# Kernel tuning notes

Measured on AMD Instinct MI355X. Metric: run time of the kernel, lower is better.

The kernel has to match this reference:

```python
import jax, jax.numpy as jnp
import numpy as np

N, D, DFF, H, L = 98280, 192, 384, 8, 36
S = N // L  # 2730 sets per partition
HD = D // H
EPS = 1e-5


def _ln(x, g, b):
    m = x.mean(-1, keepdims=True)
    v = ((x - m) ** 2).mean(-1, keepdims=True)
    return (x - m) * jax.lax.rsqrt(v + EPS) * g + b


def _mha(q, k, v, Wqkv, bqkv, Wo, bo, mask):
    # q,k,v: (S, L, D); mask: (S, L), True = padded key
    Wq, Wk, Wv = jnp.split(Wqkv, 3, axis=0)
    bq, bk, bv = jnp.split(bqkv, 3)
    qh = (q @ Wq.T + bq).reshape(S, L, H, HD)
    kh = (k @ Wk.T + bk).reshape(S, L, H, HD)
    vh = (v @ Wv.T + bv).reshape(S, L, H, HD)
    scores = jnp.einsum('slhd,smhd->shlm', qh, kh) / np.sqrt(HD).astype(np.float32)
    scores = jnp.where(mask[:, None, None, :], -1e9, scores)
    attn = jax.nn.softmax(scores, axis=-1)
    out = jnp.einsum('shlm,smhd->slhd', attn, vh).reshape(S, L, D)
    return out @ Wo.T + bo


def _layer(x, pos, inds, mask, Wqkv, bqkv, Wo, bo, W1, b1, W2, b2,
           g1, be1, g2, be2, gn, bn):
    identity = x
    sf = x[inds]                 # gather voxels into sets: (S, L, D)
    qk = sf + pos[inds]          # pos added to q and k only (value = sf)
    src2 = _mha(qk, qk, sf, Wqkv, bqkv, Wo, bo, mask)
    flat = inds.reshape(-1)
    # torch.unique(return_inverse) + flip + scatter == take FIRST occurrence
    # of each voxel id; .at[].min is deterministic under duplicates.
    perm = jnp.full((N,), flat.shape[0], jnp.int32).at[flat].min(
        jnp.arange(flat.shape[0], dtype=jnp.int32))
    src2 = src2.reshape(-1, D)[perm]   # scatter back: (N, D)
    x = _ln(x + src2, g1, be1)
    ff = jnp.maximum(x @ W1.T + b1, 0.0) @ W2.T + b2
    x = _ln(x + ff, g2, be2)
    return _ln(x + identity, gn, bn)   # DSVT_EncoderLayer residual norm


def reference(src, inds0, inds1, mask0, mask1, pos0, pos1,
              Wqkv, bqkv, Wo, bo, W1, b1, W2, b2,
              g1, be1, g2, be2, gn, bn, block_id):
    inds = (inds0, inds1)
    masks = (mask0, mask1)
    pos = (pos0, pos1)
    out = src
    for i in range(2):  # two set partitions within the shift (shift_id = block_id % 2)
        out = _layer(out, pos[i], inds[i], masks[i],
                     Wqkv[i], bqkv[i], Wo[i], bo[i],
                     W1[i], b1[i], W2[i], b2[i],
                     g1[i], be1[i], g2[i], be2[i], gn[i], bn[i])
    return out


def setup_inputs():
    key = jax.random.key(0)
    ks = jax.random.split(key, 16)
    sd = 0.02
    return {
        "src": jax.random.normal(ks[0], (N, D), jnp.float32),
        "inds0": jax.random.permutation(ks[1], N).reshape(S, L).astype(jnp.int32),
        "inds1": jax.random.permutation(ks[2], N).reshape(S, L).astype(jnp.int32),
        "mask0": jnp.zeros((S, L), bool),
        "mask1": jnp.zeros((S, L), bool),
        "pos0": jax.random.normal(ks[3], (N, D), jnp.float32),
        "pos1": jax.random.normal(ks[4], (N, D), jnp.float32),
        "Wqkv": sd * jax.random.normal(ks[5], (2, 3 * D, D), jnp.float32),
        "bqkv": jnp.zeros((2, 3 * D), jnp.float32),
        "Wo": sd * jax.random.normal(ks[6], (2, D, D), jnp.float32),
        "bo": jnp.zeros((2, D), jnp.float32),
        "W1": sd * jax.random.normal(ks[7], (2, DFF, D), jnp.float32),
        "b1": jnp.zeros((2, DFF), jnp.float32),
        "W2": sd * jax.random.normal(ks[8], (2, D, DFF), jnp.float32),
        "b2": jnp.zeros((2, D), jnp.float32),
        "g1": jnp.ones((2, D), jnp.float32),
        "be1": jnp.zeros((2, D), jnp.float32),
        "g2": jnp.ones((2, D), jnp.float32),
        "be2": jnp.zeros((2, D), jnp.float32),
        "gn": jnp.ones((2, D), jnp.float32),
        "bn": jnp.zeros((2, D), jnp.float32),
        "block_id": 0,
    }
```

## Files before the change

### kernel.cpp

```cpp
#include <hip/hip_runtime.h>
#include <stdint.h>

#define NVOX   98280
#define S_SETS 2730
#define L_SET  36
#define D_MODEL 192
#define D_FF    384
#define N_HEADS 8
#define H_DIM   24

using s16x8 = __attribute__((ext_vector_type(8))) short;
using s16x4 = __attribute__((ext_vector_type(4))) short;
using f32x4 = __attribute__((ext_vector_type(4))) float;

__device__ __forceinline__ float bf2f(unsigned short h) {
    unsigned u = ((unsigned)h) << 16;
    return __builtin_bit_cast(float, u);
}
__device__ __forceinline__ unsigned short f2bf(float f) {
    unsigned u = __builtin_bit_cast(unsigned, f);
    u += 0x7FFF + ((u >> 16) & 1);
    return (unsigned short)(u >> 16);
}

__global__ __launch_bounds__(256)
void convert_f32_bf16(const float* __restrict__ src, short* __restrict__ dst, int n)
{
    int i = blockIdx.x * 256 + threadIdx.x;
    if (i < n) dst[i] = (short)f2bf(src[i]);
}

__global__ __launch_bounds__(256)
void gather_kernel(const float* __restrict__ x, const float* __restrict__ pos,
                   const int* __restrict__ inds,
                   short* __restrict__ qk, short* __restrict__ sf)
{
    int f = blockIdx.x * 4 + (threadIdx.x >> 6);
    int lane = threadIdx.x & 63;
    if (lane >= 48) return;
    int v = inds[f];
    float4 a = *(const float4*)(x + (size_t)v * D_MODEL + lane * 4);
    float4 p = *(const float4*)(pos + (size_t)v * D_MODEL + lane * 4);
    s16x4 q, s;
    q[0] = (short)f2bf(a.x + p.x); q[1] = (short)f2bf(a.y + p.y);
    q[2] = (short)f2bf(a.z + p.z); q[3] = (short)f2bf(a.w + p.w);
    s[0] = (short)f2bf(a.x); s[1] = (short)f2bf(a.y);
    s[2] = (short)f2bf(a.z); s[3] = (short)f2bf(a.w);
    *(s16x4*)(qk + (size_t)f * D_MODEL + lane * 4) = q;
    *(s16x4*)(sf + (size_t)f * D_MODEL + lane * 4) = s;
}

__global__ __launch_bounds__(512, 4)
void qkv_direct(const short* __restrict__ qk, const short* __restrict__ sf,
                const short* __restrict__ W, const float* __restrict__ bias,
                short* __restrict__ C, int n)
{
    __shared__ char Bs[36864];
    const int bx = blockIdx.x;
    const int sec = bx >> 1, half = bx & 1;
    const int colOff = sec * 192 + half * 96;
    const short* Ap = (sec == 2) ? sf : qk;
    const short* Wp = W + (size_t)colOff * 192;
    const int rowBase = blockIdx.y * 128;
    const int tid = threadIdx.x;

    #pragma unroll
    for (int t = tid; t < 2304; t += 512) {
        int row = t / 24, c8 = t % 24;
        s16x8 v = *(const s16x8*)(Wp + (size_t)row * 192 + c8 * 8);
        *(s16x8*)(Bs + row * 384 + ((c8 * 16) ^ ((row & 7) << 4))) = v;
    }
    __syncthreads();

    const int wid = tid >> 6, lane = tid & 63;
    const int lr = lane & 15, kb = lane >> 4;
    const int arow = rowBase + wid * 16 + lr;
    const bool rv = arow < n;
    const short* Arow = Ap + (size_t)arow * 192 + kb * 8;

    f32x4 acc[6] = {};
    #pragma unroll
    for (int ks = 0; ks < 6; ++ks) {
        s16x8 a = {};
        if (rv) a = *(const s16x8*)(Arow + ks * 32);
        s16x8 b[6];
        #pragma unroll
        for (int fj = 0; fj < 6; ++fj) {
            int row = fj * 16 + lr;
            b[fj] = *(const s16x8*)(Bs + row * 384 + ((ks * 64 + kb * 16) ^ ((row & 7) << 4)));
        }
        #pragma unroll
        for (int fj = 0; fj < 6; ++fj)
            acc[fj] = __builtin_amdgcn_mfma_f32_16x16x32_bf16(a, b[fj], acc[fj], 0, 0, 0);
    }
    #pragma unroll
    for (int fj = 0; fj < 6; ++fj) {
        int col = colOff + fj * 16 + lr;
        float bv = bias[col];
        #pragma unroll
        for (int r = 0; r < 4; ++r) {
            int grow = rowBase + wid * 16 + kb * 4 + r;
            if (grow < n)
                C[(size_t)grow * 576 + col] = (short)f2bf(acc[fj][r] + bv);
        }
    }
}

__global__ __launch_bounds__(64)
void attn_mfma(const short* __restrict__ qkv, const unsigned char* __restrict__ mask,
               short* __restrict__ attn_out)
{
    const int s = blockIdx.x >> 3;
    const int h = blockIdx.x & 7;
    __shared__ short Pl[48 * 64];
    char* Pb = (char*)Pl;
    const int lane = threadIdx.x;
    const int lr = lane & 15, g = lane >> 4;

    #pragma unroll
    for (int i = 0; i < 6; ++i)
        *(s16x8*)(Pl + i * 512 + lane * 8) = (s16x8){};

    s16x8 qa[3], kb3[3];
    #pragma unroll
    for (int t = 0; t < 3; ++t) {
        int rr = t * 16 + lr;
        qa[t] = (s16x8){};
        kb3[t] = (s16x8){};
        if (rr < L_SET && g < 3) {
            const short* base = qkv + (size_t)(s * L_SET + rr) * 576 + h * H_DIM + g * 8;
            qa[t] = *(const s16x8*)(base);
            kb3[t] = *(const s16x8*)(base + 192);
        }
    }
    f32x4 sc[3][3] = {};
    #pragma unroll
    for (int mt = 0; mt < 3; ++mt)
        #pragma unroll
        for (int nt = 0; nt < 3; ++nt)
            sc[mt][nt] = __builtin_amdgcn_mfma_f32_16x16x32_bf16(qa[mt], kb3[nt], sc[mt][nt], 0, 0, 0);

    s16x8 vb[2][2];
    #pragma unroll
    for (int ks = 0; ks < 2; ++ks)
        #pragma unroll
        for (int nt = 0; nt < 2; ++nt)
            #pragma unroll
            for (int e = 0; e < 8; ++e) {
                size_t row = (size_t)s * L_SET + ks * 32 + g * 8 + e;
                vb[ks][nt][e] = qkv[row * 576 + 384 + h * H_DIM + nt * 16 + lr];
            }

    const float scale = 0.20412414523193154f;
    bool colmask[3];
    #pragma unroll
    for (int nt = 0; nt < 3; ++nt) {
        int m = nt * 16 + lr;
        colmask[nt] = (m >= L_SET) || (mask[(size_t)s * L_SET + (m < L_SET ? m : 0)] != 0);
    }
    #pragma unroll
    for (int mt = 0; mt < 3; ++mt) {
        #pragma unroll
        for (int r = 0; r < 4; ++r) {
            float v[3], ev[3];
            #pragma unroll
            for (int nt = 0; nt < 3; ++nt)
                v[nt] = colmask[nt] ? -1e9f : sc[mt][nt][r] * scale;
            float mx = fmaxf(fmaxf(v[0], v[1]), v[2]);
            #pragma unroll
            for (int off = 1; off < 16; off <<= 1) mx = fmaxf(mx, __shfl_xor(mx, off, 64));
            float sm = 0.f;
            #pragma unroll
            for (int nt = 0; nt < 3; ++nt) { ev[nt] = __expf(v[nt] - mx); sm += ev[nt]; }
            #pragma unroll
            for (int off = 1; off < 16; off <<= 1) sm += __shfl_xor(sm, off, 64);
            float rinv = 1.f / sm;
            int q = mt * 16 + g * 4 + r;
            #pragma unroll
            for (int nt = 0; nt < 3; ++nt) {
                int m = nt * 16 + lr;
                *(short*)(Pb + q * 128 + ((m * 2) ^ ((q & 7) << 4))) =
                    (short)f2bf(ev[nt] * rinv);
            }
        }
    }

    f32x4 o[3][2] = {};
    #pragma unroll
    for (int ks = 0; ks < 2; ++ks) {
        s16x8 pa[3];
        #pragma unroll
        for (int mt = 0; mt < 3; ++mt) {
            int row = mt * 16 + lr;
            pa[mt] = *(const s16x8*)(Pb + row * 128 + ((ks * 64 + g * 16) ^ ((row & 7) << 4)));
        }
        #pragma unroll
        for (int mt = 0; mt < 3; ++mt)
            #pragma unroll
            for (int nt = 0; nt < 2; ++nt)
                o[mt][nt] = __builtin_amdgcn_mfma_f32_16x16x32_bf16(pa[mt], vb[ks][nt], o[mt][nt], 0, 0, 0);
    }

    #pragma unroll
    for (int mt = 0; mt < 3; ++mt) {
        #pragma unroll
        for (int nt = 0; nt < 2; ++nt) {
            #pragma unroll
            for (int r = 0; r < 4; ++r) {
                int q = mt * 16 + g * 4 + r;
                int d = nt * 16 + lr;
                if (q < L_SET && d < H_DIM)
                    attn_out[(size_t)(s * L_SET + q) * D_MODEL + h * H_DIM + d] =
                        (short)f2bf(o[mt][nt][r]);
            }
        }
    }
}

__device__ __forceinline__ float wave_sum64(float v) {
    #pragma unroll
    for (int off = 32; off > 0; off >>= 1) v += __shfl_xor(v, off, 64);
    return v;
}

__global__ __launch_bounds__(512)
void wo_ln1(const short* __restrict__ attnb, const short* __restrict__ Wo,
            const float* __restrict__ bo, const int* __restrict__ inds,
            const float* __restrict__ xin,
            const float* __restrict__ g1, const float* __restrict__ be1,
            short* __restrict__ x1, int n)
{
    extern __shared__ char pool[];
    char* As = pool;
    char* Bs = pool + 49152;
    float* Cf = (float*)pool;
    const int rowBase = blockIdx.x * 128;
    const int tid = threadIdx.x;

    #pragma unroll
    for (int t = tid; t < 3072; t += 512) {
        int row = t / 24, c8 = t % 24;
        int grow = rowBase + row;
        s16x8 v = {};
        if (grow < n) v = *(const s16x8*)(attnb + (size_t)grow * 192 + c8 * 8);
        *(s16x8*)(As + row * 384 + ((c8 * 16) ^ ((row & 7) << 4))) = v;
    }
    #pragma unroll
    for (int t = tid; t < 4608; t += 512) {
        int row = t / 24, c8 = t % 24;
        s16x8 v = *(const s16x8*)(Wo + (size_t)row * 192 + c8 * 8);
        *(s16x8*)(Bs + row * 384 + ((c8 * 16) ^ ((row & 7) << 4))) = v;
    }
    __syncthreads();

    const int wid = tid >> 6, lane = tid & 63;
    const int lr = lane & 15, kb = lane >> 4;
    const int wm = wid & 3, wn = wid >> 2;
    f32x4 acc[2][6] = {};
    #pragma unroll
    for (int ks = 0; ks < 6; ++ks) {
        s16x8 a[2], b[6];
        #pragma unroll
        for (int fi = 0; fi < 2; ++fi) {
            int row = wm * 32 + fi * 16 + lr;
            a[fi] = *(const s16x8*)(As + row * 384 + ((ks * 64 + kb * 16) ^ ((row & 7) << 4)));
        }
        #pragma unroll
        for (int fj = 0; fj < 6; ++fj) {
            int row = wn * 96 + fj * 16 + lr;
            b[fj] = *(const s16x8*)(Bs + row * 384 + ((ks * 64 + kb * 16) ^ ((row & 7) << 4)));
        }
        #pragma unroll
        for (int fi = 0; fi < 2; ++fi)
            #pragma unroll
            for (int fj = 0; fj < 6; ++fj)
                acc[fi][fj] = __builtin_amdgcn_mfma_f32_16x16x32_bf16(a[fi], b[fj], acc[fi][fj], 0, 0, 0);
    }
    __syncthreads();
    #pragma unroll
    for (int fj = 0; fj < 6; ++fj) {
        int col = wn * 96 + fj * 16 + lr;
        float bv = bo[col];
        #pragma unroll
        for (int fi = 0; fi < 2; ++fi)
            #pragma unroll
            for (int r = 0; r < 4; ++r) {
                int row = wm * 32 + fi * 16 + kb * 4 + r;
                Cf[row * 192 + col] = acc[fi][fj][r] + bv;
            }
    }
    __syncthreads();

    int vv[16];
    #pragma unroll
    for (int i = 0; i < 16; ++i) {
        int f = rowBase + wid * 16 + i;
        vv[i] = (f < n) ? inds[f] : 0;
    }
    float4 xr[16];
    #pragma unroll
    for (int i = 0; i < 16; ++i)
        xr[i] = (lane < 48) ? *(const float4*)(xin + (size_t)vv[i] * D_MODEL + lane * 4)
                            : make_float4(0.f, 0.f, 0.f, 0.f);
    float4 gv = (lane < 48) ? *(const float4*)(g1 + lane * 4) : make_float4(0,0,0,0);
    float4 bv = (lane < 48) ? *(const float4*)(be1 + lane * 4) : make_float4(0,0,0,0);
    #pragma unroll
    for (int i = 0; i < 16; ++i) {
        int r = wid * 16 + i;
        int f = rowBase + r;
        float4 t = make_float4(0.f, 0.f, 0.f, 0.f);
        if (lane < 48) {
            float4 c4 = *(const float4*)&Cf[r * 192 + lane * 4];
            t.x = c4.x + xr[i].x; t.y = c4.y + xr[i].y;
            t.z = c4.z + xr[i].z; t.w = c4.w + xr[i].w;
        }
        float mean = wave_sum64(t.x + t.y + t.z + t.w) * (1.f / 192.f);
        float ss   = wave_sum64(t.x*t.x + t.y*t.y + t.z*t.z + t.w*t.w) * (1.f / 192.f);
        float inv = rsqrtf(ss - mean * mean + 1e-5f);
        if (lane < 48 && f < n) {
            s16x4 o;
            o[0] = (short)f2bf((t.x - mean) * inv * gv.x + bv.x);
            o[1] = (short)f2bf((t.y - mean) * inv * gv.y + bv.y);
            o[2] = (short)f2bf((t.z - mean) * inv * gv.z + bv.z);
            o[3] = (short)f2bf((t.w - mean) * inv * gv.w + bv.w);
            *(s16x4*)(x1 + (size_t)vv[i] * D_MODEL + lane * 4) = o;
        }
    }
}

__global__ __launch_bounds__(512)
void ffn_fused(const short* __restrict__ x1, const short* __restrict__ W1,
               const float* __restrict__ b1, const short* __restrict__ W2,
               const float* __restrict__ b2, const float* __restrict__ xin,
               const float* __restrict__ g2, const float* __restrict__ be2,
               const float* __restrict__ gn, const float* __restrict__ bn,
               float* __restrict__ outp, int n)
{
    extern __shared__ char pool[];
    char* Ax  = pool;
    char* W1c = pool + 49152;
    char* W2c = pool + 86016;
    char* Hc  = pool + 125952;
    float* Cf = (float*)(pool + 49152);
    const int rowBase = blockIdx.x * 128;
    const int tid = threadIdx.x;
    const int wid = tid >> 6, lane = tid & 63;
    const int lr = lane & 15, kb = lane >> 4;
    const int wm = wid & 3, wn = wid >> 2;

    #pragma unroll
    for (int t = tid; t < 3072; t += 512) {
        int row = t / 24, c8 = t % 24;
        int grow = rowBase + row;
        s16x8 v = {};
        if (grow < n) v = *(const s16x8*)(x1 + (size_t)grow * 192 + c8 * 8);
        *(s16x8*)(Ax + row * 384 + ((c8 * 16) ^ ((row & 7) << 4))) = v;
    }

    f32x4 acc2[2][6] = {};
    for (int c = 0; c < 4; ++c) {
        __syncthreads();
        #pragma unroll
        for (int t = tid; t < 2304; t += 512) {
            int row = t / 24, c8 = t % 24;
            s16x8 v = *(const s16x8*)(W1 + (size_t)(c * 96 + row) * 192 + c8 * 8);
            *(s16x8*)(W1c + row * 384 + ((c8 * 16) ^ ((row & 7) << 4))) = v;
        }
        #pragma unroll
        for (int t = tid; t < 2304; t += 512) {
            int row = t / 12, c8 = t % 12;
            s16x8 v = *(const s16x8*)(W2 + (size_t)row * 384 + c * 96 + c8 * 8);
            *(s16x8*)(W2c + row * 208 + c8 * 16) = v;
        }
        __syncthreads();
        f32x4 acc1[2][3] = {};
        #pragma unroll
        for (int ks = 0; ks < 6; ++ks) {
            s16x8 a[2], b[3];
            #pragma unroll
            for (int fi = 0; fi < 2; ++fi) {
                int row = wm * 32 + fi * 16 + lr;
                a[fi] = *(const s16x8*)(Ax + row * 384 + ((ks * 64 + kb * 16) ^ ((row & 7) << 4)));
            }
            #pragma unroll
            for (int fj = 0; fj < 3; ++fj) {
                int row = wn * 48 + fj * 16 + lr;
                b[fj] = *(const s16x8*)(W1c + row * 384 + ((ks * 64 + kb * 16) ^ ((row & 7) << 4)));
            }
            #pragma unroll
            for (int fi = 0; fi < 2; ++fi)
                #pragma unroll
                for (int fj = 0; fj < 3; ++fj)
                    acc1[fi][fj] = __builtin_amdgcn_mfma_f32_16x16x32_bf16(a[fi], b[fj], acc1[fi][fj], 0, 0, 0);
        }
        #pragma unroll
        for (int fj = 0; fj < 3; ++fj) {
            int col = wn * 48 + fj * 16 + lr;
            float b1v = b1[c * 96 + col];
            #pragma unroll
            for (int fi = 0; fi < 2; ++fi)
                #pragma unroll
                for (int r = 0; r < 4; ++r) {
                    int row = wm * 32 + fi * 16 + kb * 4 + r;
                    *(short*)(Hc + row * 208 + col * 2) =
                        (short)f2bf(fmaxf(acc1[fi][fj][r] + b1v, 0.f));
                }
        }
        __syncthreads();
        #pragma unroll
        for (int ks = 0; ks < 3; ++ks) {
            s16x8 a[2], b[6];
            #pragma unroll
            for (int fi = 0; fi < 2; ++fi) {
                int row = wm * 32 + fi * 16 + lr;
                a[fi] = *(const s16x8*)(Hc + row * 208 + ks * 64 + kb * 16);
            }
            #pragma unroll
            for (int fj = 0; fj < 6; ++fj) {
                int row = wn * 96 + fj * 16 + lr;
                b[fj] = *(const s16x8*)(W2c + row * 208 + ks * 64 + kb * 16);
            }
            #pragma unroll
            for (int fi = 0; fi < 2; ++fi)
                #pragma unroll
                for (int fj = 0; fj < 6; ++fj)
                    acc2[fi][fj] = __builtin_amdgcn_mfma_f32_16x16x32_bf16(a[fi], b[fj], acc2[fi][fj], 0, 0, 0);
        }
    }
    __syncthreads();
    #pragma unroll
    for (int fj = 0; fj < 6; ++fj) {
        int col = wn * 96 + fj * 16 + lr;
        float bv = b2[col];
        #pragma unroll
        for (int fi = 0; fi < 2; ++fi)
            #pragma unroll
            for (int r = 0; r < 4; ++r) {
                int row = wm * 32 + fi * 16 + kb * 4 + r;
                Cf[row * 192 + col] = acc2[fi][fj][r] + bv;
            }
    }
    __syncthreads();

    float4 xr[16];
    #pragma unroll
    for (int i = 0; i < 16; ++i) {
        int gvx = rowBase + wid * 16 + i;
        xr[i] = (lane < 48 && gvx < n)
              ? *(const float4*)(xin + (size_t)gvx * D_MODEL + lane * 4)
              : make_float4(0.f, 0.f, 0.f, 0.f);
    }
    float4 g2v = (lane < 48) ? *(const float4*)(g2 + lane * 4) : make_float4(0,0,0,0);
    float4 b2v = (lane < 48) ? *(const float4*)(be2 + lane * 4) : make_float4(0,0,0,0);
    float4 gnv = (lane < 48) ? *(const float4*)(gn + lane * 4) : make_float4(0,0,0,0);
    float4 bnv = (lane < 48) ? *(const float4*)(bn + lane * 4) : make_float4(0,0,0,0);
    #pragma unroll
    for (int i = 0; i < 16; ++i) {
        int r = wid * 16 + i;
        int gvx = rowBase + r;
        float4 t = make_float4(0.f, 0.f, 0.f, 0.f);
        if (lane < 48) {
            float4 f4 = *(const float4*)&Cf[r * 192 + lane * 4];
            int byteoff = r * 384 + (((lane >> 1) << 4) ^ ((r & 7) << 4)) + ((lane & 1) << 3);
            s16x4 xv = *(const s16x4*)(Ax + byteoff);
            t.x = f4.x + bf2f((unsigned short)xv[0]);
            t.y = f4.y + bf2f((unsigned short)xv[1]);
            t.z = f4.z + bf2f((unsigned short)xv[2]);
            t.w = f4.w + bf2f((unsigned short)xv[3]);
        }
        float m1 = wave_sum64(t.x + t.y + t.z + t.w) * (1.f / 192.f);
        float s1 = wave_sum64(t.x*t.x + t.y*t.y + t.z*t.z + t.w*t.w) * (1.f / 192.f);
        float i1 = rsqrtf(s1 - m1 * m1 + 1e-5f);
        float4 t2 = make_float4(0.f, 0.f, 0.f, 0.f);
        if (lane < 48) {
            t2.x = (t.x - m1) * i1 * g2v.x + b2v.x + xr[i].x;
            t2.y = (t.y - m1) * i1 * g2v.y + b2v.y + xr[i].y;
            t2.z = (t.z - m1) * i1 * g2v.z + b2v.z + xr[i].z;
            t2.w = (t.w - m1) * i1 * g2v.w + b2v.w + xr[i].w;
        }
        float m2 = wave_sum64(t2.x + t2.y + t2.z + t2.w) * (1.f / 192.f);
        float s2 = wave_sum64(t2.x*t2.x + t2.y*t2.y + t2.z*t2.z + t2.w*t2.w) * (1.f / 192.f);
        float i2 = rsqrtf(s2 - m2 * m2 + 1e-5f);
        if (lane < 48 && gvx < n) {
            float4 o;
            o.x = (t2.x - m2) * i2 * gnv.x + bnv.x;
            o.y = (t2.y - m2) * i2 * gnv.y + bnv.y;
            o.z = (t2.z - m2) * i2 * gnv.z + bnv.z;
            o.w = (t2.w - m2) * i2 * gnv.w + bnv.w;
            *(float4*)(outp + (size_t)gvx * D_MODEL + lane * 4) = o;
        }
    }
}

extern "C" void kernel_launch(void* const* d_in, const int* in_sizes, int n_in,
                              void* d_out, int out_size, void* d_ws, size_t ws_size,
                              hipStream_t stream)
{
    (void)in_sizes; (void)n_in; (void)out_size;
    const int N = NVOX;
    const float* src = (const float*)d_in[0];
    const int* inds[2] = {(const int*)d_in[1], (const int*)d_in[2]};
    const unsigned char* mask[2] = {(const unsigned char*)d_in[3], (const unsigned char*)d_in[4]};
    const float* pos[2] = {(const float*)d_in[5], (const float*)d_in[6]};
    const float* Wqkv = (const float*)d_in[7];
    const float* bqkv = (const float*)d_in[8];
    const float* Wo   = (const float*)d_in[9];
    const float* bo   = (const float*)d_in[10];
    const float* W1   = (const float*)d_in[11];
    const float* b1   = (const float*)d_in[12];
    const float* W2   = (const float*)d_in[13];
    const float* b2   = (const float*)d_in[14];
    const float* g1   = (const float*)d_in[15];
    const float* be1  = (const float*)d_in[16];
    const float* g2   = (const float*)d_in[17];
    const float* be2  = (const float*)d_in[18];
    const float* gn   = (const float*)d_in[19];
    const float* bn   = (const float*)d_in[20];

    float* out = (float*)d_out;
    short* wsS = (short*)d_ws;

    const size_t NE = (size_t)N * D_MODEL;
    short* wqkv_b = wsS;
    short* wo_b   = wsS + 221184;
    short* w1_b   = wsS + 294912;
    short* w2_b   = wsS + 442368;
    const size_t base = 1048576;
    short* qk    = wsS + base;
    short* sf    = qk + NE;
    short* qkvb  = sf + NE;
    short* attnb = qkvb + 3 * NE;
    short* x1    = attnb + NE;

    if (ws_size < (base + 7 * NE) * sizeof(short)) return;

    const dim3 blk(256);
    convert_f32_bf16<<<dim3(864), blk, 0, stream>>>(Wqkv, wqkv_b, 221184);
    convert_f32_bf16<<<dim3(288), blk, 0, stream>>>(Wo,   wo_b,   73728);
    convert_f32_bf16<<<dim3(576), blk, 0, stream>>>(W1,   w1_b,   147456);
    convert_f32_bf16<<<dim3(576), blk, 0, stream>>>(W2,   w2_b,   147456);

    const int RT = (N + 127) / 128;
    for (int i = 0; i < 2; ++i) {
        const float* xin = (i == 0) ? src : out;
        gather_kernel<<<dim3(24570), blk, 0, stream>>>(xin, pos[i], inds[i], qk, sf);
        qkv_direct<<<dim3(6, RT), dim3(512), 0, stream>>>(
            qk, sf, wqkv_b + (size_t)i * 110592, bqkv + i * 576, qkvb, N);
        attn_mfma<<<dim3(S_SETS * N_HEADS), dim3(64), 0, stream>>>(qkvb, mask[i], attnb);
        wo_ln1<<<dim3(RT), dim3(512), 122880, stream>>>(
            attnb, wo_b + (size_t)i * 36864, bo + i * 192, inds[i], xin,
            g1 + i * 192, be1 + i * 192, x1, N);
        ffn_fused<<<dim3(RT), dim3(512), 152576, stream>>>(
            x1, w1_b + (size_t)i * 73728, b1 + i * 384, w2_b + (size_t)i * 73728,
            b2 + i * 192, xin, g2 + i * 192, be2 + i * 192,
            gn + i * 192, bn + i * 192, out, N);
    }
}
```

Before: 791.1 us.

## Shrink FFN tile to 64 rows and read operands directly from global

Replaces the 128-row, 512-thread FFN kernel, which used 152 KB of LDS, with a 64-row, 256-thread kernel using 48 KB static LDS and launch bounds allowing 3 blocks per CU. Activation and weight MFMA fragments are now loaded straight from global memory (relying on L2/L1 cache hits) instead of being staged into swizzled LDS, which removes the LDS staging and its barriers. The aim is higher occupancy and less synchronisation, at the cost of more global or cache traffic for the weights, which are re-read by twice as many blocks. It also risks uncoalesced 16-byte fragment loads.

```diff
diff --git a/kernel.cpp b/kernel.cpp
--- a/kernel.cpp
+++ b/kernel.cpp
@@ -328,71 +328,46 @@
     }
 }
 
-__global__ __launch_bounds__(512)
-void ffn_fused(const short* __restrict__ x1, const short* __restrict__ W1,
-               const float* __restrict__ b1, const short* __restrict__ W2,
-               const float* __restrict__ b2, const float* __restrict__ xin,
-               const float* __restrict__ g2, const float* __restrict__ be2,
-               const float* __restrict__ gn, const float* __restrict__ bn,
-               float* __restrict__ outp, int n)
-{
-    extern __shared__ char pool[];
-    char* Ax  = pool;
-    char* W1c = pool + 49152;
-    char* W2c = pool + 86016;
-    char* Hc  = pool + 125952;
-    float* Cf = (float*)(pool + 49152);
-    const int rowBase = blockIdx.x * 128;
+__global__ __launch_bounds__(256, 3)
+void ffn64(const short* __restrict__ x1, const short* __restrict__ W1,
+           const float* __restrict__ b1, const short* __restrict__ W2,
+           const float* __restrict__ b2, const float* __restrict__ xin,
+           const float* __restrict__ g2, const float* __restrict__ be2,
+           const float* __restrict__ gn, const float* __restrict__ bn,
+           float* __restrict__ outp, int n)
+{
+    __shared__ char pool[49152];
+    char* Hc = pool;
+    float* Cf = (float*)pool;
+    const int rowBase = blockIdx.x * 64;
     const int tid = threadIdx.x;
     const int wid = tid >> 6, lane = tid & 63;
     const int lr = lane & 15, kb = lane >> 4;
-    const int wm = wid & 3, wn = wid >> 2;
-
-    #pragma unroll
-    for (int t = tid; t < 3072; t += 512) {
-        int row = t / 24, c8 = t % 24;
-        int grow = rowBase + row;
-        s16x8 v = {};
-        if (grow < n) v = *(const s16x8*)(x1 + (size_t)grow * 192 + c8 * 8);
-        *(s16x8*)(Ax + row * 384 + ((c8 * 16) ^ ((row & 7) << 4))) = v;
-    }
+    const int wm = wid & 1, wn = wid >> 1;
 
     f32x4 acc2[2][6] = {};
     for (int c = 0; c < 4; ++c) {
-        __syncthreads();
-        #pragma unroll
-        for (int t = tid; t < 2304; t += 512) {
-            int row = t / 24, c8 = t % 24;
-            s16x8 v = *(const s16x8*)(W1 + (size_t)(c * 96 + row) * 192 + c8 * 8);
-            *(s16x8*)(W1c + row * 384 + ((c8 * 16) ^ ((row & 7) << 4))) = v;
-        }
-        #pragma unroll
-        for (int t = tid; t < 2304; t += 512) {
-            int row = t / 12, c8 = t % 12;
-            s16x8 v = *(const s16x8*)(W2 + (size_t)row * 384 + c * 96 + c8 * 8);
-            *(s16x8*)(W2c + row * 208 + c8 * 16) = v;
-        }
-        __syncthreads();
         f32x4 acc1[2][3] = {};
         #pragma unroll
         for (int ks = 0; ks < 6; ++ks) {
             s16x8 a[2], b[3];
             #pragma unroll
             for (int fi = 0; fi < 2; ++fi) {
-                int row = wm * 32 + fi * 16 + lr;
-                a[fi] = *(const s16x8*)(Ax + row * 384 + ((ks * 64 + kb * 16) ^ ((row & 7) << 4)));
-            }
-            #pragma unroll
-            for (int fj = 0; fj < 3; ++fj) {
-                int row = wn * 48 + fj * 16 + lr;
-                b[fj] = *(const s16x8*)(W1c + row * 384 + ((ks * 64 + kb * 16) ^ ((row & 7) << 4)));
-            }
+                int arow = rowBase + wm * 32 + fi * 16 + lr;
+                a[fi] = (s16x8){};
+                if (arow < n)
+                    a[fi] = *(const s16x8*)(x1 + (size_t)arow * 192 + ks * 32 + kb * 8);
+            }
+            #pragma unroll
+            for (int fj = 0; fj < 3; ++fj)
+                b[fj] = *(const s16x8*)(W1 + (size_t)(c * 96 + wn * 48 + fj * 16 + lr) * 192 + ks * 32 + kb * 8);
             #pragma unroll
             for (int fi = 0; fi < 2; ++fi)
                 #pragma unroll
                 for (int fj = 0; fj < 3; ++fj)
                     acc1[fi][fj] = __builtin_amdgcn_mfma_f32_16x16x32_bf16(a[fi], b[fj], acc1[fi][fj], 0, 0, 0);
         }
+        __syncthreads();
         #pragma unroll
         for (int fj = 0; fj < 3; ++fj) {
             int col = wn * 48 + fj * 16 + lr;
@@ -416,10 +391,8 @@
                 a[fi] = *(const s16x8*)(Hc + row * 208 + ks * 64 + kb * 16);
             }
             #pragma unroll
-            for (int fj = 0; fj < 6; ++fj) {
-                int row = wn * 96 + fj * 16 + lr;
-                b[fj] = *(const s16x8*)(W2c + row * 208 + ks * 64 + kb * 16);
-            }
+            for (int fj = 0; fj < 6; ++fj)
+                b[fj] = *(const s16x8*)(W2 + (size_t)(wn * 96 + fj * 16 + lr) * 384 + c * 96 + ks * 32 + kb * 8);
             #pragma unroll
             for (int fi = 0; fi < 2; ++fi)
                 #pragma unroll
@@ -442,14 +415,6 @@
     }
     __syncthreads();
 
-    float4 xr[16];
-    #pragma unroll
-    for (int i = 0; i < 16; ++i) {
-        int gvx = rowBase + wid * 16 + i;
-        xr[i] = (lane < 48 && gvx < n)
-              ? *(const float4*)(xin + (size_t)gvx * D_MODEL + lane * 4)
-              : make_float4(0.f, 0.f, 0.f, 0.f);
-    }
     float4 g2v = (lane < 48) ? *(const float4*)(g2 + lane * 4) : make_float4(0,0,0,0);
     float4 b2v = (lane < 48) ? *(const float4*)(be2 + lane * 4) : make_float4(0,0,0,0);
     float4 gnv = (lane < 48) ? *(const float4*)(gn + lane * 4) : make_float4(0,0,0,0);
@@ -458,11 +423,13 @@
     for (int i = 0; i < 16; ++i) {
         int r = wid * 16 + i;
         int gvx = rowBase + r;
+        bool valid = (gvx < n) && (lane < 48);
         float4 t = make_float4(0.f, 0.f, 0.f, 0.f);
-        if (lane < 48) {
+        float4 xr = t;
+        if (valid) {
             float4 f4 = *(const float4*)&Cf[r * 192 + lane * 4];
-            int byteoff = r * 384 + (((lane >> 1) << 4) ^ ((r & 7) << 4)) + ((lane & 1) << 3);
-            s16x4 xv = *(const s16x4*)(Ax + byteoff);
+            s16x4 xv = *(const s16x4*)(x1 + (size_t)gvx * D_MODEL + lane * 4);
+            xr = *(const float4*)(xin + (size_t)gvx * D_MODEL + lane * 4);
             t.x = f4.x + bf2f((unsigned short)xv[0]);
             t.y = f4.y + bf2f((unsigned short)xv[1]);
             t.z = f4.z + bf2f((unsigned short)xv[2]);
@@ -472,16 +439,16 @@
         float s1 = wave_sum64(t.x*t.x + t.y*t.y + t.z*t.z + t.w*t.w) * (1.f / 192.f);
         float i1 = rsqrtf(s1 - m1 * m1 + 1e-5f);
         float4 t2 = make_float4(0.f, 0.f, 0.f, 0.f);
-        if (lane < 48) {
-            t2.x = (t.x - m1) * i1 * g2v.x + b2v.x + xr[i].x;
-            t2.y = (t.y - m1) * i1 * g2v.y + b2v.y + xr[i].y;
-            t2.z = (t.z - m1) * i1 * g2v.z + b2v.z + xr[i].z;
-            t2.w = (t.w - m1) * i1 * g2v.w + b2v.w + xr[i].w;
+        if (valid) {
+            t2.x = (t.x - m1) * i1 * g2v.x + b2v.x + xr.x;
+            t2.y = (t.y - m1) * i1 * g2v.y + b2v.y + xr.y;
+            t2.z = (t.z - m1) * i1 * g2v.z + b2v.z + xr.z;
+            t2.w = (t.w - m1) * i1 * g2v.w + b2v.w + xr.w;
         }
         float m2 = wave_sum64(t2.x + t2.y + t2.z + t2.w) * (1.f / 192.f);
         float s2 = wave_sum64(t2.x*t2.x + t2.y*t2.y + t2.z*t2.z + t2.w*t2.w) * (1.f / 192.f);
         float i2 = rsqrtf(s2 - m2 * m2 + 1e-5f);
-        if (lane < 48 && gvx < n) {
+        if (valid) {
             float4 o;
             o.x = (t2.x - m2) * i2 * gnv.x + bnv.x;
             o.y = (t2.y - m2) * i2 * gnv.y + bnv.y;
@@ -540,17 +507,18 @@
     convert_f32_bf16<<<dim3(576), blk, 0, stream>>>(W1,   w1_b,   147456);
     convert_f32_bf16<<<dim3(576), blk, 0, stream>>>(W2,   w2_b,   147456);
 
-    const int RT = (N + 127) / 128;
+    const int RT128 = (N + 127) / 128;
+    const int RT64  = (N + 63) / 64;
     for (int i = 0; i < 2; ++i) {
         const float* xin = (i == 0) ? src : out;
         gather_kernel<<<dim3(24570), blk, 0, stream>>>(xin, pos[i], inds[i], qk, sf);
-        qkv_direct<<<dim3(6, RT), dim3(512), 0, stream>>>(
+        qkv_direct<<<dim3(6, RT128), dim3(512), 0, stream>>>(
             qk, sf, wqkv_b + (size_t)i * 110592, bqkv + i * 576, qkvb, N);
         attn_mfma<<<dim3(S_SETS * N_HEADS), dim3(64), 0, stream>>>(qkvb, mask[i], attnb);
-        wo_ln1<<<dim3(RT), dim3(512), 122880, stream>>>(
+        wo_ln1<<<dim3(RT128), dim3(512), 122880, stream>>>(
             attnb, wo_b + (size_t)i * 36864, bo + i * 192, inds[i], xin,
             g1 + i * 192, be1 + i * 192, x1, N);
-        ffn_fused<<<dim3(RT), dim3(512), 152576, stream>>>(
+        ffn64<<<dim3(RT64), blk, 0, stream>>>(
             x1, w1_b + (size_t)i * 73728, b1 + i * 384, w2_b + (size_t)i * 73728,
             b2 + i * 192, xin, g2 + i * 192, be2 + i * 192,
             gn + i * 192, bn + i * 192, out, N);
```

Measured after the change: 899.8 us. 1.14x slower.
